# Kernel tuning notes

Hardware: AMD Instinct MI355X
Metric: run time of the kernel (lower is better)

The kernel has to match this reference:

```python
import jax, jax.numpy as jnp
import numpy as np

VOCAB = 100000
D = 128
B = 256
L = 2048  # leaves per tree (power of two -> complete binary tree)


def setup_inputs() -> dict:
    key = jax.random.key(0)
    k1, k2, k3, k4 = jax.random.split(key, 4)
    word_ids = jax.random.randint(k1, (B, L), 0, VOCAB)
    embedding = jax.random.normal(k2, (VOCAB, D), dtype=jnp.float32) * 0.1
    # torch nn.Linear(2*D, D): weight [D, 2*D], bias [D]
    W = jax.random.normal(k3, (D, 2 * D), dtype=jnp.float32) * (1.0 / np.sqrt(2 * D))
    b = jax.random.normal(k4, (D,), dtype=jnp.float32) * 0.01
    return {"word_ids": word_ids, "embedding": embedding, "W": W, "b": b}


def reference(word_ids, embedding, W, b):
    # Leaves: embedding lookup for every leaf of every tree. [B, L, D]
    x = embedding[word_ids]
    # Internal nodes, batched by depth: each level combines adjacent pairs
    # via linear(concat(left, right)). log2(L) levels (static unroll).
    while x.shape[1] > 1:
        left = x[:, 0::2, :]   # [B, n/2, D]
        right = x[:, 1::2, :]  # [B, n/2, D]
        pair = jnp.concatenate([left, right], axis=-1)  # [B, n/2, 2D]
        x = jnp.einsum('bnd,od->bno', pair, W) + b      # [B, n/2, D]
    return x[:, 0, :]  # root result per tree, [B, D]
```

## Files before the change

kernel.cpp:

```cpp
#include <hip/hip_runtime.h>


typedef __bf16 bf16x8 __attribute__((ext_vector_type(8)));
typedef __bf16 bf16x4 __attribute__((ext_vector_type(4)));
typedef float f32x4 __attribute__((ext_vector_type(4)));

#define STRIDE 136

#define BARRIER() do {                                          \
    asm volatile("s_waitcnt lgkmcnt(0)" ::: "memory");          \
    __builtin_amdgcn_s_barrier();                               \
} while (0)

__global__ void prep_kernel(const float* __restrict__ W,
                            const float* __restrict__ emb,
                            __bf16* __restrict__ wpack,
                            __bf16* __restrict__ etab, int n8) {
    const int tid = threadIdx.x;
    if (blockIdx.x < 16) {
        const int f = blockIdx.x;
        const int wv = tid >> 6, l = tid & 63;
        const int nl = f >> 3, kk = f & 7;
        const int o = ((wv << 1) + nl) * 16 + (l & 15);
        const int d = kk * 32 + ((l >> 4) << 3);
        const float* src = W + o * 256 + d;
        bf16x8 h;
#pragma unroll
        for (int j = 0; j < 8; ++j) h[j] = (__bf16)src[j];
        *(bf16x8*)(wpack + (size_t)(f * 256 + tid) * 8) = h;
    }
    const int stride = gridDim.x * blockDim.x;
    for (int i = blockIdx.x * blockDim.x + tid; i < n8; i += stride) {
        const float* s = emb + (size_t)i * 8;
        const f32x4 a = *(const f32x4*)s;
        const f32x4 b = *(const f32x4*)(s + 4);
        const bf16x4 ha = __builtin_convertvector(a, bf16x4);
        const bf16x4 hb = __builtin_convertvector(b, bf16x4);
        bf16x8 h;
#pragma unroll
        for (int j = 0; j < 4; ++j) { h[j] = ha[j]; h[4 + j] = hb[j]; }
        *(bf16x8*)(etab + (size_t)i * 8) = h;
    }
}

__device__ __forceinline__ void step32(
    const __bf16* src0, const __bf16* src1, __bf16* dst,
    const bf16x8* wf, const float* bval, int wv, int q, int lm)
{
    f32x4 acc[2][2];
#pragma unroll
    for (int mt = 0; mt < 2; ++mt)
#pragma unroll
        for (int nl = 0; nl < 2; ++nl)
            acc[mt][nl] = f32x4{ bval[nl], bval[nl], bval[nl], bval[nl] };
#pragma unroll
    for (int kh = 0; kh < 2; ++kh) {
        const int row = 2 * lm + kh;
        bf16x8 a0[4], a1[4];
#pragma unroll
        for (int j = 0; j < 4; ++j) {
            a0[j] = *(const bf16x8*)&src0[row * STRIDE + j * 32 + q * 8];
            a1[j] = *(const bf16x8*)&src1[row * STRIDE + j * 32 + q * 8];
        }
#pragma unroll
        for (int j = 0; j < 4; ++j) {
            acc[0][0] = __builtin_amdgcn_mfma_f32_16x16x32_bf16(
                a0[j], wf[0 * 8 + kh * 4 + j], acc[0][0], 0, 0, 0);
            acc[1][0] = __builtin_amdgcn_mfma_f32_16x16x32_bf16(
                a1[j], wf[0 * 8 + kh * 4 + j], acc[1][0], 0, 0, 0);
            acc[0][1] = __builtin_amdgcn_mfma_f32_16x16x32_bf16(
                a0[j], wf[1 * 8 + kh * 4 + j], acc[0][1], 0, 0, 0);
            acc[1][1] = __builtin_amdgcn_mfma_f32_16x16x32_bf16(
                a1[j], wf[1 * 8 + kh * 4 + j], acc[1][1], 0, 0, 0);
        }
    }
#pragma unroll
    for (int mt = 0; mt < 2; ++mt)
#pragma unroll
        for (int nl = 0; nl < 2; ++nl) {
            const int col = (2 * wv + nl) * 16 + lm;
            const bf16x4 hv = __builtin_convertvector(acc[mt][nl], bf16x4);
#pragma unroll
            for (int r = 0; r < 4; ++r)
                dst[(mt * 16 + q * 4 + r) * STRIDE + col] = hv[r];
        }
}

template <int NOUT>
__device__ __forceinline__ void step_small(
    const __bf16* src, __bf16* dst,
    const bf16x8* wf, const float* bval, int wv, int q, int lm)
{
    const int me = (NOUT >= 16) ? lm : (lm < NOUT ? lm : 0);
    f32x4 acc[2];
    acc[0] = f32x4{ bval[0], bval[0], bval[0], bval[0] };
    acc[1] = f32x4{ bval[1], bval[1], bval[1], bval[1] };
#pragma unroll
    for (int kh = 0; kh < 2; ++kh) {
        const int row = 2 * me + kh;
        bf16x8 af[4];
#pragma unroll
        for (int j = 0; j < 4; ++j)
            af[j] = *(const bf16x8*)&src[row * STRIDE + j * 32 + q * 8];
#pragma unroll
        for (int nl = 0; nl < 2; ++nl)
#pragma unroll
            for (int j = 0; j < 4; ++j)
                acc[nl] = __builtin_amdgcn_mfma_f32_16x16x32_bf16(
                    af[j], wf[nl * 8 + kh * 4 + j], acc[nl], 0, 0, 0);
    }
#pragma unroll
    for (int nl = 0; nl < 2; ++nl) {
        const int col = (2 * wv + nl) * 16 + lm;
        const bf16x4 hv = __builtin_convertvector(acc[nl], bf16x4);
#pragma unroll
        for (int r = 0; r < 4; ++r) {
            const int row = q * 4 + r;
            if (row < NOUT)
                dst[row * STRIDE + col] = hv[r];
        }
    }
}

__device__ __forceinline__ void final4(
    const __bf16* src, __bf16* yrow,
    const bf16x8* wf, const float* bval, int wv, int q, int lm)
{
    const int me = (lm < 4) ? lm : 0;
    f32x4 acc[2];
    acc[0] = f32x4{ bval[0], bval[0], bval[0], bval[0] };
    acc[1] = f32x4{ bval[1], bval[1], bval[1], bval[1] };
#pragma unroll
    for (int kh = 0; kh < 2; ++kh) {
        const int row = 2 * me + kh;
        bf16x8 af[4];
#pragma unroll
        for (int j = 0; j < 4; ++j)
            af[j] = *(const bf16x8*)&src[row * STRIDE + j * 32 + q * 8];
#pragma unroll
        for (int nl = 0; nl < 2; ++nl)
#pragma unroll
            for (int j = 0; j < 4; ++j)
                acc[nl] = __builtin_amdgcn_mfma_f32_16x16x32_bf16(
                    af[j], wf[nl * 8 + kh * 4 + j], acc[nl], 0, 0, 0);
    }
#pragma unroll
    for (int nl = 0; nl < 2; ++nl) {
        const int col = (2 * wv + nl) * 16 + lm;
        if (q == 0) {
#pragma unroll
            for (int r = 0; r < 4; ++r)
                yrow[r * 128 + col] = (__bf16)acc[nl][r];
        }
    }
}

__device__ __forceinline__ void gissue_bf(
    const int (&ids)[4], const __bf16* etab, int tid, bf16x8 (&s)[4])
{
#pragma unroll
    for (int i = 0; i < 4; ++i)
        s[i] = *(const bf16x8*)(etab + (size_t)ids[i] * 128 + (tid & 15) * 8);
}
__device__ __forceinline__ void gwrite_bf(
    __bf16* dst, int tid, const bf16x8 (&s)[4])
{
#pragma unroll
    for (int i = 0; i < 4; ++i) {
        const int row = (tid >> 4) + 16 * i;
        *(bf16x8*)&dst[row * STRIDE + (tid & 15) * 8] = s[i];
    }
}

__device__ __forceinline__ void gissue_f32(
    const int* wb64, const float* emb, int tid, f32x4 (&s)[8])
{
#pragma unroll
    for (int i = 0; i < 8; ++i) {
        const int id = wb64[(tid >> 5) + 8 * i];
        s[i] = *(const f32x4*)(emb + (size_t)id * 128 + (tid & 31) * 4);
    }
}
__device__ __forceinline__ void gwrite_f32(
    __bf16* dst, int tid, const f32x4 (&s)[8])
{
#pragma unroll
    for (int i = 0; i < 8; ++i) {
        const int row = (tid >> 5) + 8 * i;
        *(bf16x4*)&dst[row * STRIDE + (tid & 31) * 4] =
            __builtin_convertvector(s[i], bf16x4);
    }
}

template <bool BF>
__global__ __launch_bounds__(256, 3) void tree128_kernel(
    const int* __restrict__ wid, const float* __restrict__ emb,
    const __bf16* __restrict__ etab, const __bf16* __restrict__ wpack,
    const float* __restrict__ bias, __bf16* __restrict__ yout)
{
    __shared__ __align__(16) __bf16 bufA[64 * STRIDE];
    __shared__ __align__(16) __bf16 bufB[64 * STRIDE];
    __shared__ __align__(16) __bf16 bufD[64 * STRIDE];
    const int tid = threadIdx.x;
    const int batch = blockIdx.x >> 3;
    const int pair = blockIdx.x & 7;
    const int wv = tid >> 6, ln = tid & 63, q = ln >> 4, lm = ln & 15;

    bf16x8 wf[16];
    const bf16x8* wp = (const bf16x8*)wpack;
#pragma unroll
    for (int f = 0; f < 16; ++f) wf[f] = wp[f * 256 + tid];
    float bval[2];
    bval[0] = bias[(2 * wv + 0) * 16 + lm];
    bval[1] = bias[(2 * wv + 1) * 16 + lm];

    const int* wb = wid + batch * 2048 + pair * 256;

    if constexpr (BF) {
        int ids[4][4];
#pragma unroll
        for (int g = 0; g < 4; ++g)
#pragma unroll
            for (int i = 0; i < 4; ++i)
                ids[g][i] = wb[g * 64 + (tid >> 4) + 16 * i];

        bf16x8 s1[4], s2[4];
        gissue_bf(ids[0], etab, tid, s1);
        gissue_bf(ids[1], etab, tid, s2);
        gwrite_bf(bufA, tid, s1);
        BARRIER();
        gissue_bf(ids[2], etab, tid, s1);
        step32(bufA, bufA + 32 * STRIDE, bufB, wf, bval, wv, q, lm);
        BARRIER();
        gwrite_bf(bufA, tid, s2);
        BARRIER();
        gissue_bf(ids[3], etab, tid, s2);
        step32(bufA, bufA + 32 * STRIDE, bufB + 32 * STRIDE, wf, bval, wv, q, lm);
        BARRIER();
        gwrite_bf(bufA, tid, s1);
        step32(bufB, bufB + 32 * STRIDE, bufD, wf, bval, wv, q, lm);
        BARRIER();
        step32(bufA, bufA + 32 * STRIDE, bufB, wf, bval, wv, q, lm);
        BARRIER();
        gwrite_bf(bufA, tid, s2);
        BARRIER();
        step32(bufA, bufA + 32 * STRIDE, bufB + 32 * STRIDE, wf, bval, wv, q, lm);
        BARRIER();
    } else {
        f32x4 st[8];
        gissue_f32(wb, emb, tid, st);
        gwrite_f32(bufA, tid, st);
        BARRIER();
        gissue_f32(wb + 64, emb, tid, st);
        step32(bufA, bufA + 32 * STRIDE, bufB, wf, bval, wv, q, lm);
        BARRIER();
        gwrite_f32(bufA, tid, st);
        BARRIER();
        gissue_f32(wb + 128, emb, tid, st);
        step32(bufA, bufA + 32 * STRIDE, bufB + 32 * STRIDE, wf, bval, wv, q, lm);
        BARRIER();
        gwrite_f32(bufA, tid, st);
        step32(bufB, bufB + 32 * STRIDE, bufD, wf, bval, wv, q, lm);
        BARRIER();
        step32(bufA, bufA + 32 * STRIDE, bufB, wf, bval, wv, q, lm);
        BARRIER();
        gissue_f32(wb + 192, emb, tid, st);
        gwrite_f32(bufA, tid, st);
        BARRIER();
        step32(bufA, bufA + 32 * STRIDE, bufB + 32 * STRIDE, wf, bval, wv, q, lm);
        BARRIER();
    }
    step32(bufB, bufB + 32 * STRIDE, bufD + 32 * STRIDE, wf, bval, wv, q, lm);
    BARRIER();
    step32(bufD, bufD + 32 * STRIDE, bufB, wf, bval, wv, q, lm);
    BARRIER();
    step_small<16>(bufB, bufD, wf, bval, wv, q, lm);
    BARRIER();
    step_small<8>(bufD, bufB, wf, bval, wv, q, lm);
    BARRIER();
    final4(bufB, yout + (size_t)(batch * 32 + pair * 4) * 128,
           wf, bval, wv, q, lm);
}

__global__ __launch_bounds__(256) void tree32_kernel(
    const __bf16* __restrict__ yin, const __bf16* __restrict__ wpack,
    const float* __restrict__ bias, float* __restrict__ out)
{
    __shared__ __align__(16) __bf16 buf0[32 * STRIDE];
    __shared__ __align__(16) __bf16 buf1[16 * STRIDE];
    const int tid = threadIdx.x;
    const int batch = blockIdx.x;
    const int wv = tid >> 6, ln = tid & 63, q = ln >> 4, lm = ln & 15;

    bf16x8 wf[16];
    const bf16x8* wp = (const bf16x8*)wpack;
#pragma unroll
    for (int f = 0; f < 16; ++f) wf[f] = wp[f * 256 + tid];
    float bval[2];
    bval[0] = bias[(2 * wv + 0) * 16 + lm];
    bval[1] = bias[(2 * wv + 1) * 16 + lm];

#pragma unroll
    for (int i = 0; i < 2; ++i) {
        const int flat = tid + 256 * i;
        const int row = flat >> 4;
        const int c8 = flat & 15;
        const bf16x8 v =
            *(const bf16x8*)(yin + (size_t)(batch * 32 + row) * 128 + c8 * 8);
        *(bf16x8*)&buf0[row * STRIDE + c8 * 8] = v;
    }
    __syncthreads();

    step_small<16>(buf0, buf1, wf, bval, wv, q, lm);  __syncthreads();
    step_small<8> (buf1, buf0, wf, bval, wv, q, lm);  __syncthreads();
    step_small<4> (buf0, buf1, wf, bval, wv, q, lm);  __syncthreads();
    step_small<2> (buf1, buf0, wf, bval, wv, q, lm);  __syncthreads();

    {
        f32x4 acc[2];
        acc[0] = f32x4{ bval[0], bval[0], bval[0], bval[0] };
        acc[1] = f32x4{ bval[1], bval[1], bval[1], bval[1] };
#pragma unroll
        for (int kh = 0; kh < 2; ++kh) {
            bf16x8 af[4];
#pragma unroll
            for (int j = 0; j < 4; ++j)
                af[j] = *(const bf16x8*)&buf0[kh * STRIDE + j * 32 + q * 8];
#pragma unroll
            for (int nl = 0; nl < 2; ++nl)
#pragma unroll
                for (int j = 0; j < 4; ++j)
                    acc[nl] = __builtin_amdgcn_mfma_f32_16x16x32_bf16(
                        af[j], wf[nl * 8 + kh * 4 + j], acc[nl], 0, 0, 0);
        }
#pragma unroll
        for (int nl = 0; nl < 2; ++nl) {
            const int col = (2 * wv + nl) * 16 + lm;
            if (q == 0) out[(size_t)batch * 128 + col] = acc[nl][0];
        }
    }
}

extern "C" void kernel_launch(void* const* d_in, const int* in_sizes, int n_in,
                              void* d_out, int out_size, void* d_ws, size_t ws_size,
                              hipStream_t stream) {
    const int*   wid = (const int*)d_in[0];
    const float* emb = (const float*)d_in[1];
    const float* W   = (const float*)d_in[2];
    const float* b   = (const float*)d_in[3];
    float* out = (float*)d_out;

    __bf16* wpack = (__bf16*)d_ws;
    __bf16* y     = wpack + 32768;
    __bf16* etab  = y + 256 * 32 * 128;

    const size_t need = (size_t)32768 * 2 + (size_t)256 * 32 * 128 * 2
                      + (size_t)100000 * 128 * 2;
    const bool bf = (ws_size >= need);
    const int n8 = bf ? (100000 * 128 / 8) : 0;

    prep_kernel<<<bf ? 2048 : 16, 256, 0, stream>>>(W, emb, wpack, etab, n8);
    if (bf)
        tree128_kernel<true><<<2048, 256, 0, stream>>>(
            wid, emb, etab, wpack, b, y);
    else
        tree128_kernel<false><<<2048, 256, 0, stream>>>(
            wid, emb, etab, wpack, b, y);
    tree32_kernel<<<256, 256, 0, stream>>>(y, wpack, b, out);
}
```

Measured before the change: 130.7 us.

## Fuse pairs of tree levels into one linear map over four children

Because the tree combine is linear, two consecutive levels are collapsed into a single 4-child linear map. The weight W2 [128x512] = [W_L W_L, W_L W_R, W_R W_L, W_R W_R] and bias b2 = b + (W_L+W_R) b are precomputed in the prep kernel. The tree kernels then do half as many levels, which halves the barriers and LDS round trips, and the leaf gather order is changed to group quads. In exchange, per-level MFMA work per output doubles in K, half of W2 is streamed from global or L2 instead of registers, the prep step gains a serial 128-step product per thread, and bf16 rounding of the composed weights changes numerics slightly.

After: 158.3 us. +21.1%, slower.

```diff
diff --git a/kernel.cpp b/kernel.cpp
--- a/kernel.cpp
+++ b/kernel.cpp
@@ -13,24 +13,54 @@
 } while (0)
 
 __global__ void prep_kernel(const float* __restrict__ W,
+                            const float* __restrict__ bias,
                             const float* __restrict__ emb,
-                            __bf16* __restrict__ wpack,
+                            __bf16* __restrict__ wpack1,
+                            __bf16* __restrict__ wpack2,
+                            float* __restrict__ b2,
                             __bf16* __restrict__ etab, int n8) {
     const int tid = threadIdx.x;
-    if (blockIdx.x < 16) {
-        const int f = blockIdx.x;
-        const int wv = tid >> 6, l = tid & 63;
-        const int nl = f >> 3, kk = f & 7;
+    const int bx = blockIdx.x;
+    const int wv = tid >> 6, l = tid & 63;
+    if (bx < 16) {
+        const int nl = bx >> 3, kk = bx & 7;
         const int o = ((wv << 1) + nl) * 16 + (l & 15);
         const int d = kk * 32 + ((l >> 4) << 3);
         const float* src = W + o * 256 + d;
         bf16x8 h;
 #pragma unroll
         for (int j = 0; j < 8; ++j) h[j] = (__bf16)src[j];
-        *(bf16x8*)(wpack + (size_t)(f * 256 + tid) * 8) = h;
+        *(bf16x8*)(wpack1 + (size_t)(bx * 256 + tid) * 8) = h;
+    } else if (bx < 48) {
+        const int f2 = bx - 16;
+        const int nl = f2 >> 4, kk = f2 & 15;
+        const int o = ((wv << 1) + nl) * 16 + (l & 15);
+        const int d = kk * 32 + ((l >> 4) << 3);
+        const int s = d >> 7, c = d & 127;
+        const float* wrow = W + o * 256 + (s >> 1) * 128;
+        const float* wcol = W + (s & 1) * 128 + c;
+        float a8[8] = {0, 0, 0, 0, 0, 0, 0, 0};
+        for (int k = 0; k < 128; ++k) {
+            const float wl = wrow[k];
+            const float* wr = wcol + k * 256;
+#pragma unroll
+            for (int j = 0; j < 8; ++j) a8[j] += wl * wr[j];
+        }
+        bf16x8 h;
+#pragma unroll
+        for (int j = 0; j < 8; ++j) h[j] = (__bf16)a8[j];
+        *(bf16x8*)(wpack2 + (size_t)(f2 * 256 + tid) * 8) = h;
+    } else if (bx == 48) {
+        if (tid < 128) {
+            float acc = bias[tid];
+            const float* wr = W + tid * 256;
+            for (int k = 0; k < 128; ++k)
+                acc += (wr[k] + wr[128 + k]) * bias[k];
+            b2[tid] = acc;
+        }
     }
     const int stride = gridDim.x * blockDim.x;
-    for (int i = blockIdx.x * blockDim.x + tid; i < n8; i += stride) {
+    for (int i = bx * blockDim.x + tid; i < n8; i += stride) {
         const float* s = emb + (size_t)i * 8;
         const f32x4 a = *(const f32x4*)s;
         const f32x4 b = *(const f32x4*)(s + 4);
@@ -43,160 +73,87 @@
     }
 }
 
-__device__ __forceinline__ void step32(
-    const __bf16* src0, const __bf16* src1, __bf16* dst,
-    const bf16x8* wf, const float* bval, int wv, int q, int lm)
-{
-    f32x4 acc[2][2];
-#pragma unroll
-    for (int mt = 0; mt < 2; ++mt)
-#pragma unroll
-        for (int nl = 0; nl < 2; ++nl)
-            acc[mt][nl] = f32x4{ bval[nl], bval[nl], bval[nl], bval[nl] };
-#pragma unroll
-    for (int kh = 0; kh < 2; ++kh) {
-        const int row = 2 * lm + kh;
-        bf16x8 a0[4], a1[4];
-#pragma unroll
-        for (int j = 0; j < 4; ++j) {
-            a0[j] = *(const bf16x8*)&src0[row * STRIDE + j * 32 + q * 8];
-            a1[j] = *(const bf16x8*)&src1[row * STRIDE + j * 32 + q * 8];
-        }
-#pragma unroll
-        for (int j = 0; j < 4; ++j) {
-            acc[0][0] = __builtin_amdgcn_mfma_f32_16x16x32_bf16(
-                a0[j], wf[0 * 8 + kh * 4 + j], acc[0][0], 0, 0, 0);
-            acc[1][0] = __builtin_amdgcn_mfma_f32_16x16x32_bf16(
-                a1[j], wf[0 * 8 + kh * 4 + j], acc[1][0], 0, 0, 0);
-            acc[0][1] = __builtin_amdgcn_mfma_f32_16x16x32_bf16(
-                a0[j], wf[1 * 8 + kh * 4 + j], acc[0][1], 0, 0, 0);
-            acc[1][1] = __builtin_amdgcn_mfma_f32_16x16x32_bf16(
-                a1[j], wf[1 * 8 + kh * 4 + j], acc[1][1], 0, 0, 0);
-        }
-    }
-#pragma unroll
-    for (int mt = 0; mt < 2; ++mt)
-#pragma unroll
-        for (int nl = 0; nl < 2; ++nl) {
-            const int col = (2 * wv + nl) * 16 + lm;
-            const bf16x4 hv = __builtin_convertvector(acc[mt][nl], bf16x4);
-#pragma unroll
-            for (int r = 0; r < 4; ++r)
-                dst[(mt * 16 + q * 4 + r) * STRIDE + col] = hv[r];
-        }
-}
-
 template <int NOUT>
-__device__ __forceinline__ void step_small(
-    const __bf16* src, __bf16* dst,
-    const bf16x8* wf, const float* bval, int wv, int q, int lm)
+__device__ __forceinline__ void quad_acc_stream(
+    const __bf16* src, const bf16x8* wres, const bf16x8* wp2,
+    const float* b2v, int tid, int q, int lm, f32x4 (&acc)[2])
 {
     const int me = (NOUT >= 16) ? lm : (lm < NOUT ? lm : 0);
-    f32x4 acc[2];
-    acc[0] = f32x4{ bval[0], bval[0], bval[0], bval[0] };
-    acc[1] = f32x4{ bval[1], bval[1], bval[1], bval[1] };
-#pragma unroll
-    for (int kh = 0; kh < 2; ++kh) {
-        const int row = 2 * me + kh;
-        bf16x8 af[4];
-#pragma unroll
-        for (int j = 0; j < 4; ++j)
-            af[j] = *(const bf16x8*)&src[row * STRIDE + j * 32 + q * 8];
-#pragma unroll
-        for (int nl = 0; nl < 2; ++nl)
-#pragma unroll
-            for (int j = 0; j < 4; ++j)
-                acc[nl] = __builtin_amdgcn_mfma_f32_16x16x32_bf16(
-                    af[j], wf[nl * 8 + kh * 4 + j], acc[nl], 0, 0, 0);
-    }
-#pragma unroll
-    for (int nl = 0; nl < 2; ++nl) {
-        const int col = (2 * wv + nl) * 16 + lm;
-        const bf16x4 hv = __builtin_convertvector(acc[nl], bf16x4);
-#pragma unroll
-        for (int r = 0; r < 4; ++r) {
-            const int row = q * 4 + r;
-            if (row < NOUT)
-                dst[row * STRIDE + col] = hv[r];
-        }
-    }
-}
-
-__device__ __forceinline__ void final4(
-    const __bf16* src, __bf16* yrow,
-    const bf16x8* wf, const float* bval, int wv, int q, int lm)
-{
-    const int me = (lm < 4) ? lm : 0;
-    f32x4 acc[2];
-    acc[0] = f32x4{ bval[0], bval[0], bval[0], bval[0] };
-    acc[1] = f32x4{ bval[1], bval[1], bval[1], bval[1] };
-#pragma unroll
-    for (int kh = 0; kh < 2; ++kh) {
-        const int row = 2 * me + kh;
-        bf16x8 af[4];
-#pragma unroll
-        for (int j = 0; j < 4; ++j)
-            af[j] = *(const bf16x8*)&src[row * STRIDE + j * 32 + q * 8];
-#pragma unroll
-        for (int nl = 0; nl < 2; ++nl)
-#pragma unroll
-            for (int j = 0; j < 4; ++j)
-                acc[nl] = __builtin_amdgcn_mfma_f32_16x16x32_bf16(
-                    af[j], wf[nl * 8 + kh * 4 + j], acc[nl], 0, 0, 0);
-    }
-#pragma unroll
-    for (int nl = 0; nl < 2; ++nl) {
-        const int col = (2 * wv + nl) * 16 + lm;
-        if (q == 0) {
-#pragma unroll
-            for (int r = 0; r < 4; ++r)
-                yrow[r * 128 + col] = (__bf16)acc[nl][r];
-        }
+    acc[0] = f32x4{ b2v[0], b2v[0], b2v[0], b2v[0] };
+    acc[1] = f32x4{ b2v[1], b2v[1], b2v[1], b2v[1] };
+#pragma unroll
+    for (int kk = 0; kk < 16; ++kk) {
+        const bf16x8 af = *(const bf16x8*)
+            &src[((kk >> 2) * NOUT + me) * STRIDE + (kk & 3) * 32 + q * 8];
+        acc[0] = __builtin_amdgcn_mfma_f32_16x16x32_bf16(
+            af, wres[kk], acc[0], 0, 0, 0);
+        acc[1] = __builtin_amdgcn_mfma_f32_16x16x32_bf16(
+            af, wp2[(16 + kk) * 256 + tid], acc[1], 0, 0, 0);
+    }
+}
+
+template <int NOUT>
+__device__ __forceinline__ void quad_acc_res(
+    const __bf16* src, const bf16x8* w2r,
+    const float* b2v, int q, int lm, f32x4 (&acc)[2])
+{
+    const int me = (NOUT >= 16) ? lm : (lm < NOUT ? lm : 0);
+    acc[0] = f32x4{ b2v[0], b2v[0], b2v[0], b2v[0] };
+    acc[1] = f32x4{ b2v[1], b2v[1], b2v[1], b2v[1] };
+#pragma unroll
+    for (int kk = 0; kk < 16; ++kk) {
+        const bf16x8 af = *(const bf16x8*)
+            &src[((kk >> 2) * NOUT + me) * STRIDE + (kk & 3) * 32 + q * 8];
+        acc[0] = __builtin_amdgcn_mfma_f32_16x16x32_bf16(
+            af, w2r[kk], acc[0], 0, 0, 0);
+        acc[1] = __builtin_amdgcn_mfma_f32_16x16x32_bf16(
+            af, w2r[16 + kk], acc[1], 0, 0, 0);
     }
 }
 
 __device__ __forceinline__ void gissue_bf(
-    const int (&ids)[4], const __bf16* etab, int tid, bf16x8 (&s)[4])
+    const int (&ids)[4], const __bf16* etab, int tid, bf16x8 (&st)[4])
 {
 #pragma unroll
     for (int i = 0; i < 4; ++i)
-        s[i] = *(const bf16x8*)(etab + (size_t)ids[i] * 128 + (tid & 15) * 8);
+        st[i] = *(const bf16x8*)(etab + (size_t)ids[i] * 128 + (tid & 15) * 8);
 }
 __device__ __forceinline__ void gwrite_bf(
-    __bf16* dst, int tid, const bf16x8 (&s)[4])
+    __bf16* dst, int tid, const bf16x8 (&st)[4])
 {
 #pragma unroll
     for (int i = 0; i < 4; ++i) {
-        const int row = (tid >> 4) + 16 * i;
-        *(bf16x8*)&dst[row * STRIDE + (tid & 15) * 8] = s[i];
+        const int row = 16 * i + (tid >> 4);
+        *(bf16x8*)&dst[row * STRIDE + (tid & 15) * 8] = st[i];
     }
 }
 
 __device__ __forceinline__ void gissue_f32(
-    const int* wb64, const float* emb, int tid, f32x4 (&s)[8])
+    const int* wb64, const float* emb, int tid, f32x4 (&st)[8])
 {
 #pragma unroll
     for (int i = 0; i < 8; ++i) {
-        const int id = wb64[(tid >> 5) + 8 * i];
-        s[i] = *(const f32x4*)(emb + (size_t)id * 128 + (tid & 31) * 4);
+        const int rt = (tid >> 5) + 8 * i;
+        const int id = wb64[4 * (rt & 15) + (rt >> 4)];
+        st[i] = *(const f32x4*)(emb + (size_t)id * 128 + (tid & 31) * 4);
     }
 }
 __device__ __forceinline__ void gwrite_f32(
-    __bf16* dst, int tid, const f32x4 (&s)[8])
+    __bf16* dst, int tid, const f32x4 (&st)[8])
 {
 #pragma unroll
     for (int i = 0; i < 8; ++i) {
-        const int row = (tid >> 5) + 8 * i;
-        *(bf16x4*)&dst[row * STRIDE + (tid & 31) * 4] =
-            __builtin_convertvector(s[i], bf16x4);
+        const int rt = (tid >> 5) + 8 * i;
+        *(bf16x4*)&dst[rt * STRIDE + (tid & 31) * 4] =
+            __builtin_convertvector(st[i], bf16x4);
     }
 }
 
 template <bool BF>
 __global__ __launch_bounds__(256, 3) void tree128_kernel(
     const int* __restrict__ wid, const float* __restrict__ emb,
-    const __bf16* __restrict__ etab, const __bf16* __restrict__ wpack,
-    const float* __restrict__ bias, __bf16* __restrict__ yout)
+    const __bf16* __restrict__ etab, const __bf16* __restrict__ wpack2,
+    const float* __restrict__ b2, __bf16* __restrict__ yout)
 {
     __shared__ __align__(16) __bf16 bufA[64 * STRIDE];
     __shared__ __align__(16) __bf16 bufB[64 * STRIDE];
@@ -206,45 +163,53 @@
     const int pair = blockIdx.x & 7;
     const int wv = tid >> 6, ln = tid & 63, q = ln >> 4, lm = ln & 15;
 
-    bf16x8 wf[16];
-    const bf16x8* wp = (const bf16x8*)wpack;
-#pragma unroll
-    for (int f = 0; f < 16; ++f) wf[f] = wp[f * 256 + tid];
-    float bval[2];
-    bval[0] = bias[(2 * wv + 0) * 16 + lm];
-    bval[1] = bias[(2 * wv + 1) * 16 + lm];
+    const bf16x8* wp2 = (const bf16x8*)wpack2;
+    bf16x8 wres[16];
+#pragma unroll
+    for (int f = 0; f < 16; ++f) wres[f] = wp2[f * 256 + tid];
+    float b2v[2];
+    b2v[0] = b2[(2 * wv + 0) * 16 + lm];
+    b2v[1] = b2[(2 * wv + 1) * 16 + lm];
 
     const int* wb = wid + batch * 2048 + pair * 256;
+
+    auto L12 = [&](const __bf16* src, int c) {
+        f32x4 a2[2];
+        quad_acc_stream<16>(src, wres, wp2, b2v, tid, q, lm, a2);
+#pragma unroll
+        for (int nl = 0; nl < 2; ++nl) {
+            const int col = (2 * wv + nl) * 16 + lm;
+            const bf16x4 hv = __builtin_convertvector(a2[nl], bf16x4);
+#pragma unroll
+            for (int r = 0; r < 4; ++r)
+                bufD[(r * 16 + 4 * c + q) * STRIDE + col] = hv[r];
+        }
+    };
 
     if constexpr (BF) {
         int ids[4][4];
 #pragma unroll
-        for (int g = 0; g < 4; ++g)
+        for (int c = 0; c < 4; ++c)
 #pragma unroll
             for (int i = 0; i < 4; ++i)
-                ids[g][i] = wb[g * 64 + (tid >> 4) + 16 * i];
-
+                ids[c][i] = wb[64 * c + 4 * (tid >> 4) + i];
         bf16x8 s1[4], s2[4];
         gissue_bf(ids[0], etab, tid, s1);
         gissue_bf(ids[1], etab, tid, s2);
         gwrite_bf(bufA, tid, s1);
         BARRIER();
         gissue_bf(ids[2], etab, tid, s1);
-        step32(bufA, bufA + 32 * STRIDE, bufB, wf, bval, wv, q, lm);
-        BARRIER();
-        gwrite_bf(bufA, tid, s2);
+        L12(bufA, 0);
+        gwrite_bf(bufB, tid, s2);
         BARRIER();
         gissue_bf(ids[3], etab, tid, s2);
-        step32(bufA, bufA + 32 * STRIDE, bufB + 32 * STRIDE, wf, bval, wv, q, lm);
-        BARRIER();
+        L12(bufB, 1);
         gwrite_bf(bufA, tid, s1);
-        step32(bufB, bufB + 32 * STRIDE, bufD, wf, bval, wv, q, lm);
-        BARRIER();
-        step32(bufA, bufA + 32 * STRIDE, bufB, wf, bval, wv, q, lm);
-        BARRIER();
-        gwrite_bf(bufA, tid, s2);
-        BARRIER();
-        step32(bufA, bufA + 32 * STRIDE, bufB + 32 * STRIDE, wf, bval, wv, q, lm);
+        BARRIER();
+        L12(bufA, 2);
+        gwrite_bf(bufB, tid, s2);
+        BARRIER();
+        L12(bufB, 3);
         BARRIER();
     } else {
         f32x4 st[8];
@@ -252,74 +217,120 @@
         gwrite_f32(bufA, tid, st);
         BARRIER();
         gissue_f32(wb + 64, emb, tid, st);
-        step32(bufA, bufA + 32 * STRIDE, bufB, wf, bval, wv, q, lm);
-        BARRIER();
+        L12(bufA, 0);
+        gwrite_f32(bufB, tid, st);
+        BARRIER();
+        gissue_f32(wb + 128, emb, tid, st);
+        L12(bufB, 1);
         gwrite_f32(bufA, tid, st);
         BARRIER();
-        gissue_f32(wb + 128, emb, tid, st);
-        step32(bufA, bufA + 32 * STRIDE, bufB + 32 * STRIDE, wf, bval, wv, q, lm);
-        BARRIER();
-        gwrite_f32(bufA, tid, st);
-        step32(bufB, bufB + 32 * STRIDE, bufD, wf, bval, wv, q, lm);
-        BARRIER();
-        step32(bufA, bufA + 32 * STRIDE, bufB, wf, bval, wv, q, lm);
-        BARRIER();
         gissue_f32(wb + 192, emb, tid, st);
-        gwrite_f32(bufA, tid, st);
-        BARRIER();
-        step32(bufA, bufA + 32 * STRIDE, bufB + 32 * STRIDE, wf, bval, wv, q, lm);
-        BARRIER();
-    }
-    step32(bufB, bufB + 32 * STRIDE, bufD + 32 * STRIDE, wf, bval, wv, q, lm);
+        L12(bufA, 2);
+        gwrite_f32(bufB, tid, st);
+        BARRIER();
+        L12(bufB, 3);
+        BARRIER();
+    }
+
+    {
+        f32x4 a2[2];
+        quad_acc_stream<16>(bufD, wres, wp2, b2v, tid, q, lm, a2);
+#pragma unroll
+        for (int nl = 0; nl < 2; ++nl) {
+            const int col = (2 * wv + nl) * 16 + lm;
+            const bf16x4 hv = __builtin_convertvector(a2[nl], bf16x4);
+#pragma unroll
+            for (int r = 0; r < 4; ++r)
+                bufA[(r * 4 + q) * STRIDE + col] = hv[r];
+        }
+    }
     BARRIER();
-    step32(bufD, bufD + 32 * STRIDE, bufB, wf, bval, wv, q, lm);
-    BARRIER();
-    step_small<16>(bufB, bufD, wf, bval, wv, q, lm);
-    BARRIER();
-    step_small<8>(bufD, bufB, wf, bval, wv, q, lm);
-    BARRIER();
-    final4(bufB, yout + (size_t)(batch * 32 + pair * 4) * 128,
-           wf, bval, wv, q, lm);
+    {
+        f32x4 a2[2];
+        quad_acc_stream<4>(bufA, wres, wp2, b2v, tid, q, lm, a2);
+        __bf16* yrow = yout + (size_t)(batch * 32 + pair * 4) * 128;
+#pragma unroll
+        for (int nl = 0; nl < 2; ++nl) {
+            const int col = (2 * wv + nl) * 16 + lm;
+            if (q == 0) {
+#pragma unroll
+                for (int r = 0; r < 4; ++r)
+                    yrow[r * 128 + col] = (__bf16)a2[nl][r];
+            }
+        }
+    }
 }
 
 __global__ __launch_bounds__(256) void tree32_kernel(
-    const __bf16* __restrict__ yin, const __bf16* __restrict__ wpack,
+    const __bf16* __restrict__ yin, const __bf16* __restrict__ wpack1,
+    const __bf16* __restrict__ wpack2, const float* __restrict__ b2,
     const float* __restrict__ bias, float* __restrict__ out)
 {
     __shared__ __align__(16) __bf16 buf0[32 * STRIDE];
-    __shared__ __align__(16) __bf16 buf1[16 * STRIDE];
+    __shared__ __align__(16) __bf16 buf1[8 * STRIDE];
     const int tid = threadIdx.x;
     const int batch = blockIdx.x;
     const int wv = tid >> 6, ln = tid & 63, q = ln >> 4, lm = ln & 15;
 
-    bf16x8 wf[16];
-    const bf16x8* wp = (const bf16x8*)wpack;
-#pragma unroll
-    for (int f = 0; f < 16; ++f) wf[f] = wp[f * 256 + tid];
-    float bval[2];
-    bval[0] = bias[(2 * wv + 0) * 16 + lm];
-    bval[1] = bias[(2 * wv + 1) * 16 + lm];
+    bf16x8 w2r[32];
+    const bf16x8* wp2 = (const bf16x8*)wpack2;
+#pragma unroll
+    for (int f = 0; f < 32; ++f) w2r[f] = wp2[f * 256 + tid];
+    bf16x8 w1r[16];
+    const bf16x8* wp1 = (const bf16x8*)wpack1;
+#pragma unroll
+    for (int f = 0; f < 16; ++f) w1r[f] = wp1[f * 256 + tid];
+    float b2v[2], b1v[2];
+    b2v[0] = b2[(2 * wv + 0) * 16 + lm];
+    b2v[1] = b2[(2 * wv + 1) * 16 + lm];
+    b1v[0] = bias[(2 * wv + 0) * 16 + lm];
+    b1v[1] = bias[(2 * wv + 1) * 16 + lm];
 
 #pragma unroll
     for (int i = 0; i < 2; ++i) {
         const int flat = tid + 256 * i;
-        const int row = flat >> 4;
+        const int o = flat >> 4;
         const int c8 = flat & 15;
         const bf16x8 v =
-            *(const bf16x8*)(yin + (size_t)(batch * 32 + row) * 128 + c8 * 8);
-        *(bf16x8*)&buf0[row * STRIDE + c8 * 8] = v;
+            *(const bf16x8*)(yin + (size_t)(batch * 32 + o) * 128 + c8 * 8);
+        *(bf16x8*)&buf0[((o & 3) * 8 + (o >> 2)) * STRIDE + c8 * 8] = v;
     }
     __syncthreads();
 
-    step_small<16>(buf0, buf1, wf, bval, wv, q, lm);  __syncthreads();
-    step_small<8> (buf1, buf0, wf, bval, wv, q, lm);  __syncthreads();
-    step_small<4> (buf0, buf1, wf, bval, wv, q, lm);  __syncthreads();
-    step_small<2> (buf1, buf0, wf, bval, wv, q, lm);  __syncthreads();
-
+    {
+        f32x4 a2[2];
+        quad_acc_res<8>(buf0, w2r, b2v, q, lm, a2);
+#pragma unroll
+        for (int nl = 0; nl < 2; ++nl) {
+            const int col = (2 * wv + nl) * 16 + lm;
+            const bf16x4 hv = __builtin_convertvector(a2[nl], bf16x4);
+            if (q < 2) {
+#pragma unroll
+                for (int r = 0; r < 4; ++r)
+                    buf1[(r * 2 + q) * STRIDE + col] = hv[r];
+            }
+        }
+    }
+    __syncthreads();
+    {
+        f32x4 a2[2];
+        quad_acc_res<2>(buf1, w2r, b2v, q, lm, a2);
+#pragma unroll
+        for (int nl = 0; nl < 2; ++nl) {
+            const int col = (2 * wv + nl) * 16 + lm;
+            const bf16x4 hv = __builtin_convertvector(a2[nl], bf16x4);
+            if (q == 0) {
+#pragma unroll
+                for (int r = 0; r < 2; ++r)
+                    buf0[r * STRIDE + col] = hv[r];
+            }
+        }
+    }
+    __syncthreads();
     {
         f32x4 acc[2];
-        acc[0] = f32x4{ bval[0], bval[0], bval[0], bval[0] };
-        acc[1] = f32x4{ bval[1], bval[1], bval[1], bval[1] };
+        acc[0] = f32x4{ b1v[0], b1v[0], b1v[0], b1v[0] };
+        acc[1] = f32x4{ b1v[1], b1v[1], b1v[1], b1v[1] };
 #pragma unroll
         for (int kh = 0; kh < 2; ++kh) {
             bf16x8 af[4];
@@ -331,7 +342,7 @@
 #pragma unroll
                 for (int j = 0; j < 4; ++j)
                     acc[nl] = __builtin_amdgcn_mfma_f32_16x16x32_bf16(
-                        af[j], wf[nl * 8 + kh * 4 + j], acc[nl], 0, 0, 0);
+                        af[j], w1r[nl * 8 + kh * 4 + j], acc[nl], 0, 0, 0);
         }
 #pragma unroll
         for (int nl = 0; nl < 2; ++nl) {
@@ -350,21 +361,25 @@
     const float* b   = (const float*)d_in[3];
     float* out = (float*)d_out;
 
-    __bf16* wpack = (__bf16*)d_ws;
-    __bf16* y     = wpack + 32768;
-    __bf16* etab  = y + 256 * 32 * 128;
-
-    const size_t need = (size_t)32768 * 2 + (size_t)256 * 32 * 128 * 2
-                      + (size_t)100000 * 128 * 2;
-    const bool bf = (ws_size >= need);
+    __bf16* wpack1 = (__bf16*)d_ws;
+    __bf16* wpack2 = wpack1 + 32768;
+    float*  b2     = (float*)(wpack2 + 65536);
+    __bf16* y      = (__bf16*)(b2 + 128);
+    __bf16* etab   = y + 256 * 32 * 128;
+
+    const size_t need_full = (size_t)(32768 + 65536) * 2 + 512
+                           + (size_t)256 * 32 * 128 * 2
+                           + (size_t)100000 * 128 * 2;
+    const bool bf = (ws_size >= need_full);
     const int n8 = bf ? (100000 * 128 / 8) : 0;
 
-    prep_kernel<<<bf ? 2048 : 16, 256, 0, stream>>>(W, emb, wpack, etab, n8);
+    prep_kernel<<<2048, 256, 0, stream>>>(W, b, emb, wpack1, wpack2, b2,
+                                          etab, n8);
     if (bf)
         tree128_kernel<true><<<2048, 256, 0, stream>>>(
-            wid, emb, etab, wpack, b, y);
+            wid, emb, etab, wpack2, b2, y);
     else
         tree128_kernel<false><<<2048, 256, 0, stream>>>(
-            wid, emb, etab, wpack, b, y);
-    tree32_kernel<<<256, 256, 0, stream>>>(y, wpack, b, out);
-}
+            wid, emb, etab, wpack2, b2, y);
+    tree32_kernel<<<256, 256, 0, stream>>>(y, wpack1, wpack2, b2, b, out);
+}
```
